# Kernel optimization log

Hardware: AMD Instinct MI355X
Metric: run time of the kernel (lower is better)

The kernel has to match this reference:

```python
import jax, jax.numpy as jnp
import numpy as np

K_ORDER = 3
GRID_N = 10
GRID_LO, GRID_HI = -2.0, 2.0
LAYERS = [(49, 256), (256, 256), (256, 10)]
NCOEF = GRID_N + K_ORDER  # 13


def mish(x):
    return x * jnp.tanh(jax.nn.softplus(x))


def bspline_basis(x):
    # x: (B, in) -> basis (B, in, GRID_N + K_ORDER)
    h = (GRID_HI - GRID_LO) / GRID_N
    knots = GRID_LO + h * jnp.arange(-K_ORDER, GRID_N + K_ORDER + 1, dtype=x.dtype)  # (G+2k+1,)
    xx = x[..., None]
    B = ((xx >= knots[:-1]) & (xx < knots[1:])).astype(x.dtype)  # degree-0, (B,in,G+2k)
    for d in range(1, K_ORDER + 1):
        left = (xx - knots[: -(d + 1)]) / (knots[d:-1] - knots[: -(d + 1)]) * B[..., :-1]
        right = (knots[d + 1:] - xx) / (knots[d + 1:] - knots[1:-d]) * B[..., 1:]
        B = left + right
    return B  # (B, in, G+k)


def kan_layer(x, coef, scale_base, scale_sp, bias):
    # x: (B,in); coef: (in,out,G+k); scales: (in,out); bias: (out,)
    basis = bspline_basis(x)                                   # (B,in,G+k)
    spline = jnp.einsum('big,iog->bo', basis, coef * scale_sp[..., None])
    base = jnp.einsum('bi,io->bo', mish(x), scale_base)
    return base + spline + bias


def setup_inputs() -> dict:
    key = jax.random.key(0)
    ks = jax.random.split(key, 1 + 4 * len(LAYERS))
    inp = {'x': jax.random.normal(ks[0], (8192, 1, 28, 28), dtype=jnp.float32)}
    i = 1
    for li, (fin, fout) in enumerate(LAYERS, start=1):
        inp[f'coef{li}'] = 0.1 * jax.random.normal(ks[i], (fin, fout, NCOEF), dtype=jnp.float32); i += 1
        inp[f'sb{li}'] = 1.0 + 0.1 * jax.random.normal(ks[i], (fin, fout), dtype=jnp.float32); i += 1
        inp[f'sp{li}'] = 1.0 + 0.1 * jax.random.normal(ks[i], (fin, fout), dtype=jnp.float32); i += 1
        inp[f'b{li}'] = jnp.zeros((fout,), dtype=jnp.float32); i += 1
    return inp


def reference(x, coef1, sb1, sp1, b1, coef2, sb2, sp2, b2, coef3, sb3, sp3, b3):
    B = x.shape[0]
    # avg_pool2d(x, 4): 28x28 -> 7x7
    h = x.reshape(B, 1, 7, 4, 7, 4).mean(axis=(3, 5))
    h = h.reshape(B, 49)
    h = kan_layer(h, coef1, sb1, sp1, b1)
    h = kan_layer(h, coef2, sb2, sp2, b2)
    h = kan_layer(h, coef3, sb3, sp3, b3)
    return jax.nn.log_softmax(h, axis=1)
```

## Files before the change

### kernel.cpp

```cpp
#include <hip/hip_runtime.h>
#include <hip/hip_bf16.h>

typedef __bf16 bf16x8_t __attribute__((ext_vector_type(8)));
typedef float f32x4_t __attribute__((ext_vector_type(4)));
using bf16 = __hip_bfloat16;

__device__ __forceinline__ unsigned short f2bf_bits(float v) {
  __hip_bfloat16 h = __float2bfloat16(v);
  return *reinterpret_cast<unsigned short*>(&h);
}

__device__ __forceinline__ float mish_f(float x) {
  float z = __expf(x);
  float n = z * (z + 2.0f);
  float m = x * n / (n + 2.0f);
  return (x > 10.0f) ? x : m;
}

__device__ __forceinline__ void kan_feats28(bf16* dst, float x) {
  unsigned int* d32 = (unsigned int*)dst;
#pragma unroll
  for (int d = 0; d < 7; ++d) d32[d] = 0u;
  float t = (x + 3.2f) * 2.5f;
  if (t >= 0.0f && t < 16.0f) {
    float tf = floorf(t);
    int c = (int)tf;
    float u = t - tf;
    float um = 1.0f - u;
    float u2 = u * u, u3 = u2 * u;
    const float s6 = 1.0f / 6.0f;
    float w0 = um * um * um * s6;
    float w1 = (3.0f * u3 - 6.0f * u2 + 4.0f) * s6;
    float w2 = (-3.0f * u3 + 3.0f * u2 + 3.0f * u + 1.0f) * s6;
    float w3 = u3 * s6;
    int j0 = c - 3;
    if (j0 >= 0)               dst[j0]     = __float2bfloat16(w0);
    if (j0 >= -1 && j0 <= 11)  dst[j0 + 1] = __float2bfloat16(w1);
    if (j0 >= -2 && j0 <= 10)  dst[j0 + 2] = __float2bfloat16(w2);
    if (j0 <= 9)               dst[j0 + 3] = __float2bfloat16(w3);
  }
  dst[13] = __float2bfloat16(mish_f(x));
}

__global__ __launch_bounds__(256) void prep_all(
    const float* __restrict__ c1, const float* __restrict__ sb1, const float* __restrict__ sp1,
    const float* __restrict__ c2, const float* __restrict__ sb2, const float* __restrict__ sp2,
    const float* __restrict__ c3, const float* __restrict__ sb3, const float* __restrict__ sp3,
    bf16* __restrict__ W1f, bf16* __restrict__ W2f, bf16* __restrict__ W3f) {
  const int b = blockIdx.x, t = threadIdx.x;
  float vals[14];
  if (b < 49) {
    const int i = b, o = t;
    const int ntg = o >> 4, lrr = o & 15;
    const size_t io = (size_t)i * 256 + o;
    const float spv = sp1[io];
#pragma unroll
    for (int r = 0; r < 13; ++r) vals[r] = c1[io * 13 + r] * spv;
    vals[13] = sb1[io];
#pragma unroll
    for (int d = 0; d < 7; ++d) {
      const int k2 = i * 14 + 2 * d;
      const int s = k2 >> 5, r2 = k2 & 31;
      const size_t off = ((size_t)(s * 16 + ntg)) * 512 + lrr * 32 + (r2 >> 3) * 8 + (r2 & 7);
      *(unsigned int*)(W1f + off) = (unsigned int)f2bf_bits(vals[2 * d]) |
                                    ((unsigned int)f2bf_bits(vals[2 * d + 1]) << 16);
    }
  } else if (b == 49) {
    const int ntg = t >> 4, lrr = t & 15;
#pragma unroll
    for (int d = 0; d < 9; ++d) {
      const int k2 = 686 + 2 * d;
      const int r2 = k2 & 31;
      *(unsigned int*)(W1f + ((size_t)(21 * 16 + ntg)) * 512 + lrr * 32 + (r2 >> 3) * 8 + (r2 & 7)) = 0u;
    }
  } else if (b < 562) {
    if (t >= 128) return;
    const int idx = b - 50;
    const int i = idx >> 1;
    const int o = (idx & 1) * 128 + t;
    const int ntg = o >> 4, lrr = o & 15;
    const size_t io = (size_t)i * 256 + o;
    const float spv = sp2[io];
#pragma unroll
    for (int r = 0; r < 13; ++r) vals[r] = c2[io * 13 + r] * spv;
    vals[13] = sb2[io];
#pragma unroll
    for (int d = 0; d < 7; ++d) {
      const int k2 = i * 14 + 2 * d;
      const int s = k2 >> 5, r2 = k2 & 31;
      const size_t off = ((size_t)(s * 16 + ntg)) * 512 + lrr * 32 + (r2 >> 3) * 8 + (r2 & 7);
      *(unsigned int*)(W2f + off) = (unsigned int)f2bf_bits(vals[2 * d]) |
                                    ((unsigned int)f2bf_bits(vals[2 * d + 1]) << 16);
    }
  } else {
    const int i = b - 562, o = t;
    if (o < 10) {
      const size_t io = (size_t)i * 10 + o;
      const float spv = sp3[io];
#pragma unroll
      for (int r = 0; r < 13; ++r) vals[r] = c3[io * 13 + r] * spv;
      vals[13] = sb3[io];
#pragma unroll
      for (int d = 0; d < 7; ++d) {
        const int k2 = i * 14 + 2 * d;
        const int s = k2 >> 5, r2 = k2 & 31;
        const size_t off = (size_t)s * 512 + o * 32 + (r2 >> 3) * 8 + (r2 & 7);
        *(unsigned int*)(W3f + off) = (unsigned int)f2bf_bits(vals[2 * d]) |
                                      ((unsigned int)f2bf_bits(vals[2 * d + 1]) << 16);
      }
    } else if (o < 16) {
#pragma unroll
      for (int d = 0; d < 7; ++d) {
        const int k2 = i * 14 + 2 * d;
        const int s = k2 >> 5, r2 = k2 & 31;
        *(unsigned int*)(W3f + (size_t)s * 512 + o * 32 + (r2 >> 3) * 8 + (r2 & 7)) = 0u;
      }
    }
  }
}

__global__ __launch_bounds__(1024, 4) void meganet(
    const float* __restrict__ x, const bf16* __restrict__ W1f,
    const bf16* __restrict__ W2f, const bf16* __restrict__ W3f,
    const float* __restrict__ b1, const float* __restrict__ b2,
    const float* __restrict__ b3, float* __restrict__ out) {
  __shared__ __align__(16) char lds[73728];
  float* const Hs = (float*)lds;
  bf16* const Ach0 = (bf16*)(lds + 36864);
  bf16* const Ach1 = (bf16*)(lds + 51712);
  float* const P = (float*)(lds + 66560);
  float* const xs = (float*)lds;
  float* const Red = (float*)(lds + 36864);
  float* const V = (float*)(lds + 51712);

  const int t = threadIdx.x;
  const int w = t >> 6, lane = t & 63, quad = lane >> 4, lr = lane & 15;
  const int tr = (t >> 4) & 31, ej = t & 15;
  const int r0 = blockIdx.x * 32;
  const int foff = lr * 32 + quad * 8;
  const bool cons = (w < 8);
  const int ntg0 = 2 * w;

  for (int h = 0; h < 2; ++h) {
    const float4* src = (const float4*)x + (size_t)(r0 + h * 16) * 196;
    float4* xd = (float4*)xs;
#pragma unroll
    for (int l = 0; l < 4; ++l) {
      const int idx = t + l * 1024;
      if (idx < 3136) xd[idx] = src[idx];
    }
    __syncthreads();
    if (t < 784) {
      const int img = t / 49, p = t - img * 49;
      const int oh = p / 7, ow = p - oh * 7;
      const float* xi = xs + img * 784 + oh * 112 + ow * 4;
      float s = 0.f;
#pragma unroll
      for (int rr = 0; rr < 4; ++rr)
#pragma unroll
        for (int cc = 0; cc < 4; ++cc) s += xi[rr * 28 + cc];
      P[(h * 16 + img) * 56 + p] = s * (1.0f / 16.0f);
    }
    __syncthreads();
  }

  f32x4_t acc[2][2];
#pragma unroll
  for (int m = 0; m < 2; ++m)
#pragma unroll
    for (int n = 0; n < 2; ++n) acc[m][n] = (f32x4_t){0.f, 0.f, 0.f, 0.f};

  bf16x8_t q0[4], q1[4];
  if (cons) {
#pragma unroll
    for (int s = 0; s < 4; ++s) {
      q0[s] = *(const bf16x8_t*)(W1f + (size_t)(s * 16 + ntg0) * 512 + foff);
      q1[s] = *(const bf16x8_t*)(W1f + (size_t)(s * 16 + ntg0 + 1) * 512 + foff);
    }
  } else {
    kan_feats28(Ach0 + tr * 232 + ej * 14, P[tr * 56 + ej]);
  }
  __syncthreads();
#pragma unroll
  for (int c = 0; c < 4; ++c) {
    const bf16* const Ac = (c & 1) ? Ach1 : Ach0;
    bf16* const An = (c & 1) ? Ach0 : Ach1;
    if (cons) {
      const int nks = (c < 3) ? 7 : 1;
#pragma unroll
      for (int ks = 0; ks < 7; ++ks) {
        if (ks >= nks) continue;
        const int kk = c * 7 + ks;
        const int sl = kk & 3;
        bf16x8_t bb0 = q0[sl], bb1 = q1[sl];
        if (kk + 4 < 22) {
          q0[sl] = *(const bf16x8_t*)(W1f + (size_t)((kk + 4) * 16 + ntg0) * 512 + foff);
          q1[sl] = *(const bf16x8_t*)(W1f + (size_t)((kk + 4) * 16 + ntg0 + 1) * 512 + foff);
        }
#pragma unroll
        for (int m = 0; m < 2; ++m) {
          bf16x8_t a = *(const bf16x8_t*)(Ac + (m * 16 + lr) * 232 + ks * 32 + quad * 8);
          acc[m][0] = __builtin_amdgcn_mfma_f32_16x16x32_bf16(a, bb0, acc[m][0], 0, 0, 0);
          acc[m][1] = __builtin_amdgcn_mfma_f32_16x16x32_bf16(a, bb1, acc[m][1], 0, 0, 0);
        }
      }
    } else {
      if (c < 2) {
        kan_feats28(An + tr * 232 + ej * 14, P[tr * 56 + (c + 1) * 16 + ej]);
      } else if (c == 2) {
        if (ej == 0) kan_feats28(An + tr * 232, P[tr * 56 + 48]);
        else if (ej == 1) {
          unsigned int* z = (unsigned int*)(An + tr * 232 + 14);
#pragma unroll
          for (int d = 0; d < 9; ++d) z[d] = 0u;
        }
      }
    }
    __syncthreads();
  }
  if (cons) {
#pragma unroll
    for (int m = 0; m < 2; ++m)
#pragma unroll
      for (int n = 0; n < 2; ++n) {
        const int col = w * 32 + n * 16 + lr;
        const float bn = b1[col];
        f32x4_t v;
#pragma unroll
        for (int r = 0; r < 4; ++r) v[r] = acc[m][n][r] + bn;
        *(f32x4_t*)(Hs + col * 36 + m * 16 + quad * 4) = v;
      }
  }
  __syncthreads();

#pragma unroll
  for (int m = 0; m < 2; ++m)
#pragma unroll
    for (int n = 0; n < 2; ++n) acc[m][n] = (f32x4_t){0.f, 0.f, 0.f, 0.f};
  if (cons) {
#pragma unroll
    for (int s = 0; s < 4; ++s) {
      q0[s] = *(const bf16x8_t*)(W2f + (size_t)(s * 16 + ntg0) * 512 + foff);
      q1[s] = *(const bf16x8_t*)(W2f + (size_t)(s * 16 + ntg0 + 1) * 512 + foff);
    }
  } else {
    kan_feats28(Ach0 + tr * 232 + ej * 14, Hs[ej * 36 + tr]);
  }
  __syncthreads();
#pragma unroll
  for (int c = 0; c < 16; ++c) {
    const bf16* const Ac = (c & 1) ? Ach1 : Ach0;
    bf16* const An = (c & 1) ? Ach0 : Ach1;
    if (cons) {
#pragma unroll
      for (int ks = 0; ks < 7; ++ks) {
        const int kk = c * 7 + ks;
        const int sl = kk & 3;
        bf16x8_t bb0 = q0[sl], bb1 = q1[sl];
        if (kk + 4 < 112) {
          q0[sl] = *(const bf16x8_t*)(W2f + (size_t)((kk + 4) * 16 + ntg0) * 512 + foff);
          q1[sl] = *(const bf16x8_t*)(W2f + (size_t)((kk + 4) * 16 + ntg0 + 1) * 512 + foff);
        }
#pragma unroll
        for (int m = 0; m < 2; ++m) {
          bf16x8_t a = *(const bf16x8_t*)(Ac + (m * 16 + lr) * 232 + ks * 32 + quad * 8);
          acc[m][0] = __builtin_amdgcn_mfma_f32_16x16x32_bf16(a, bb0, acc[m][0], 0, 0, 0);
          acc[m][1] = __builtin_amdgcn_mfma_f32_16x16x32_bf16(a, bb1, acc[m][1], 0, 0, 0);
        }
      }
    } else if (c < 15) {
      kan_feats28(An + tr * 232 + ej * 14, Hs[((c + 1) * 16 + ej) * 36 + tr]);
    }
    __syncthreads();
  }
  if (cons) {
#pragma unroll
    for (int m = 0; m < 2; ++m)
#pragma unroll
      for (int n = 0; n < 2; ++n) {
        const int col = w * 32 + n * 16 + lr;
        const float bn = b2[col];
        f32x4_t v;
#pragma unroll
        for (int r = 0; r < 4; ++r) v[r] = acc[m][n][r] + bn;
        *(f32x4_t*)(Hs + col * 36 + m * 16 + quad * 4) = v;
      }
  }
  __syncthreads();

  f32x4_t acc3[2];
  acc3[0] = (f32x4_t){0.f, 0.f, 0.f, 0.f};
  acc3[1] = acc3[0];
  bf16x8_t q3[4];
  if (w < 7) {
#pragma unroll
    for (int s = 0; s < 4; ++s)
      q3[s] = *(const bf16x8_t*)(W3f + (size_t)(s * 7 + w) * 512 + foff);
  } else if (!cons) {
    kan_feats28(Ach0 + tr * 232 + ej * 14, Hs[ej * 36 + tr]);
  }
  __syncthreads();
#pragma unroll
  for (int c = 0; c < 16; ++c) {
    const bf16* const Ac = (c & 1) ? Ach1 : Ach0;
    bf16* const An = (c & 1) ? Ach0 : Ach1;
    if (w < 7) {
      bf16x8_t bb = q3[c & 3];
      if (c + 4 < 16)
        q3[c & 3] = *(const bf16x8_t*)(W3f + (size_t)((c + 4) * 7 + w) * 512 + foff);
#pragma unroll
      for (int m = 0; m < 2; ++m) {
        bf16x8_t a = *(const bf16x8_t*)(Ac + (m * 16 + lr) * 232 + w * 32 + quad * 8);
        acc3[m] = __builtin_amdgcn_mfma_f32_16x16x32_bf16(a, bb, acc3[m], 0, 0, 0);
      }
    } else if (!cons && c < 15) {
      kan_feats28(An + tr * 232 + ej * 14, Hs[((c + 1) * 16 + ej) * 36 + tr]);
    }
    __syncthreads();
  }
  if (w < 7) {
#pragma unroll
    for (int m = 0; m < 2; ++m)
#pragma unroll
      for (int r = 0; r < 4; ++r)
        Red[w * 512 + (m * 16 + quad * 4 + r) * 16 + lr] = acc3[m][r];
  }
  __syncthreads();
  if (t < 512) {
    float s = (ej < 10) ? b3[ej] : 0.f;
#pragma unroll
    for (int ks = 0; ks < 7; ++ks) s += Red[ks * 512 + tr * 16 + ej];
    V[tr * 16 + ej] = s;
  }
  __syncthreads();
  if (t < 32) {
    float vv[10];
#pragma unroll
    for (int o = 0; o < 10; ++o) vv[o] = V[t * 16 + o];
    float mx = vv[0];
#pragma unroll
    for (int o = 1; o < 10; ++o) mx = fmaxf(mx, vv[o]);
    float se = 0.f;
#pragma unroll
    for (int o = 0; o < 10; ++o) se += expf(vv[o] - mx);
    const float l = mx + logf(se);
#pragma unroll
    for (int o = 0; o < 10; ++o) out[(size_t)(r0 + t) * 10 + o] = vv[o] - l;
  }
}

extern "C" void kernel_launch(void* const* d_in, const int* in_sizes, int n_in,
                              void* d_out, int out_size, void* d_ws, size_t ws_size,
                              hipStream_t stream) {
  const float* x = (const float*)d_in[0];
  const float* coef1 = (const float*)d_in[1];
  const float* sb1 = (const float*)d_in[2];
  const float* sp1 = (const float*)d_in[3];
  const float* b1 = (const float*)d_in[4];
  const float* coef2 = (const float*)d_in[5];
  const float* sb2 = (const float*)d_in[6];
  const float* sp2 = (const float*)d_in[7];
  const float* b2 = (const float*)d_in[8];
  const float* coef3 = (const float*)d_in[9];
  const float* sb3 = (const float*)d_in[10];
  const float* sp3 = (const float*)d_in[11];
  const float* b3 = (const float*)d_in[12];
  float* out = (float*)d_out;

  char* ws = (char*)d_ws;
  bf16* W1f = (bf16*)ws;
  bf16* W2f = (bf16*)(ws + 360448);
  bf16* W3f = (bf16*)(ws + 2195456);

  prep_all<<<818, 256, 0, stream>>>(coef1, sb1, sp1, coef2, sb2, sp2,
                                    coef3, sb3, sp3, W1f, W2f, W3f);
  meganet<<<256, 1024, 0, stream>>>(x, W1f, W2f, W3f, b1, b2, b3, out);
}
```

Before: 140.3 us.

## Pool input directly from global memory and use lighter barriers with MFMA priority

The input pooling stage now reads each 4x4 window straight from global memory with nontemporal vector loads, replacing the LDS staging and two extra barriers per half-batch. All __syncthreads calls become a custom barrier that waits only on LDS counters, so in-flight global weight prefetches are not drained at every barrier. MFMA consumer waves raise their scheduling priority during the matmul loops. The custom barrier relies on global-load results being waited on elsewhere by the compiler, and setprio could starve the feature-producing waves.

```diff
diff --git a/kernel.cpp b/kernel.cpp
--- a/kernel.cpp
+++ b/kernel.cpp
@@ -15,6 +15,12 @@
   float n = z * (z + 2.0f);
   float m = x * n / (n + 2.0f);
   return (x > 10.0f) ? x : m;
+}
+
+__device__ __forceinline__ void bar() {
+  asm volatile("s_waitcnt lgkmcnt(0)" ::: "memory");
+  __builtin_amdgcn_s_barrier();
+  asm volatile("" ::: "memory");
 }
 
 __device__ __forceinline__ void kan_feats28(bf16* dst, float x) {
@@ -129,7 +135,6 @@
   bf16* const Ach0 = (bf16*)(lds + 36864);
   bf16* const Ach1 = (bf16*)(lds + 51712);
   float* const P = (float*)(lds + 66560);
-  float* const xs = (float*)lds;
   float* const Red = (float*)(lds + 36864);
   float* const V = (float*)(lds + 51712);
 
@@ -141,35 +146,6 @@
   const bool cons = (w < 8);
   const int ntg0 = 2 * w;
 
-  for (int h = 0; h < 2; ++h) {
-    const float4* src = (const float4*)x + (size_t)(r0 + h * 16) * 196;
-    float4* xd = (float4*)xs;
-#pragma unroll
-    for (int l = 0; l < 4; ++l) {
-      const int idx = t + l * 1024;
-      if (idx < 3136) xd[idx] = src[idx];
-    }
-    __syncthreads();
-    if (t < 784) {
-      const int img = t / 49, p = t - img * 49;
-      const int oh = p / 7, ow = p - oh * 7;
-      const float* xi = xs + img * 784 + oh * 112 + ow * 4;
-      float s = 0.f;
-#pragma unroll
-      for (int rr = 0; rr < 4; ++rr)
-#pragma unroll
-        for (int cc = 0; cc < 4; ++cc) s += xi[rr * 28 + cc];
-      P[(h * 16 + img) * 56 + p] = s * (1.0f / 16.0f);
-    }
-    __syncthreads();
-  }
-
-  f32x4_t acc[2][2];
-#pragma unroll
-  for (int m = 0; m < 2; ++m)
-#pragma unroll
-    for (int n = 0; n < 2; ++n) acc[m][n] = (f32x4_t){0.f, 0.f, 0.f, 0.f};
-
   bf16x8_t q0[4], q1[4];
   if (cons) {
 #pragma unroll
@@ -177,15 +153,41 @@
       q0[s] = *(const bf16x8_t*)(W1f + (size_t)(s * 16 + ntg0) * 512 + foff);
       q1[s] = *(const bf16x8_t*)(W1f + (size_t)(s * 16 + ntg0 + 1) * 512 + foff);
     }
-  } else {
-    kan_feats28(Ach0 + tr * 232 + ej * 14, P[tr * 56 + ej]);
-  }
-  __syncthreads();
+  }
+
+  {
+    const float* xb = x + (size_t)r0 * 784;
+#pragma unroll
+    for (int j = t; j < 1568; j += 1024) {
+      const int img = j / 49;
+      const int p = j - img * 49;
+      const int oh = p / 7, ow = p - oh * 7;
+      const float* xi = xb + img * 784 + oh * 112 + ow * 4;
+      const f32x4_t a = __builtin_nontemporal_load((const f32x4_t*)(xi));
+      const f32x4_t b = __builtin_nontemporal_load((const f32x4_t*)(xi + 28));
+      const f32x4_t c = __builtin_nontemporal_load((const f32x4_t*)(xi + 56));
+      const f32x4_t d = __builtin_nontemporal_load((const f32x4_t*)(xi + 84));
+      const float s = (a[0] + a[1] + a[2] + a[3]) + (b[0] + b[1] + b[2] + b[3]) +
+                      (c[0] + c[1] + c[2] + c[3]) + (d[0] + d[1] + d[2] + d[3]);
+      P[img * 56 + p] = s * 0.0625f;
+    }
+  }
+  bar();
+
+  f32x4_t acc[2][2];
+#pragma unroll
+  for (int m = 0; m < 2; ++m)
+#pragma unroll
+    for (int n = 0; n < 2; ++n) acc[m][n] = (f32x4_t){0.f, 0.f, 0.f, 0.f};
+
+  if (!cons) kan_feats28(Ach0 + tr * 232 + ej * 14, P[tr * 56 + ej]);
+  bar();
 #pragma unroll
   for (int c = 0; c < 4; ++c) {
     const bf16* const Ac = (c & 1) ? Ach1 : Ach0;
     bf16* const An = (c & 1) ? Ach0 : Ach1;
     if (cons) {
+      __builtin_amdgcn_s_setprio(1);
       const int nks = (c < 3) ? 7 : 1;
 #pragma unroll
       for (int ks = 0; ks < 7; ++ks) {
@@ -204,6 +206,7 @@
           acc[m][1] = __builtin_amdgcn_mfma_f32_16x16x32_bf16(a, bb1, acc[m][1], 0, 0, 0);
         }
       }
+      __builtin_amdgcn_s_setprio(0);
     } else {
       if (c < 2) {
         kan_feats28(An + tr * 232 + ej * 14, P[tr * 56 + (c + 1) * 16 + ej]);
@@ -216,7 +219,7 @@
         }
       }
     }
-    __syncthreads();
+    bar();
   }
   if (cons) {
 #pragma unroll
@@ -231,7 +234,7 @@
         *(f32x4_t*)(Hs + col * 36 + m * 16 + quad * 4) = v;
       }
   }
-  __syncthreads();
+  bar();
 
 #pragma unroll
   for (int m = 0; m < 2; ++m)
@@ -246,12 +249,13 @@
   } else {
     kan_feats28(Ach0 + tr * 232 + ej * 14, Hs[ej * 36 + tr]);
   }
-  __syncthreads();
+  bar();
 #pragma unroll
   for (int c = 0; c < 16; ++c) {
     const bf16* const Ac = (c & 1) ? Ach1 : Ach0;
     bf16* const An = (c & 1) ? Ach0 : Ach1;
     if (cons) {
+      __builtin_amdgcn_s_setprio(1);
 #pragma unroll
       for (int ks = 0; ks < 7; ++ks) {
         const int kk = c * 7 + ks;
@@ -268,10 +272,11 @@
           acc[m][1] = __builtin_amdgcn_mfma_f32_16x16x32_bf16(a, bb1, acc[m][1], 0, 0, 0);
         }
       }
+      __builtin_amdgcn_s_setprio(0);
     } else if (c < 15) {
       kan_feats28(An + tr * 232 + ej * 14, Hs[((c + 1) * 16 + ej) * 36 + tr]);
     }
-    __syncthreads();
+    bar();
   }
   if (cons) {
 #pragma unroll
@@ -286,7 +291,7 @@
         *(f32x4_t*)(Hs + col * 36 + m * 16 + quad * 4) = v;
       }
   }
-  __syncthreads();
+  bar();
 
   f32x4_t acc3[2];
   acc3[0] = (f32x4_t){0.f, 0.f, 0.f, 0.f};
@@ -299,12 +304,13 @@
   } else if (!cons) {
     kan_feats28(Ach0 + tr * 232 + ej * 14, Hs[ej * 36 + tr]);
   }
-  __syncthreads();
+  bar();
 #pragma unroll
   for (int c = 0; c < 16; ++c) {
     const bf16* const Ac = (c & 1) ? Ach1 : Ach0;
     bf16* const An = (c & 1) ? Ach0 : Ach1;
     if (w < 7) {
+      __builtin_amdgcn_s_setprio(1);
       bf16x8_t bb = q3[c & 3];
       if (c + 4 < 16)
         q3[c & 3] = *(const bf16x8_t*)(W3f + (size_t)((c + 4) * 7 + w) * 512 + foff);
@@ -313,10 +319,11 @@
         bf16x8_t a = *(const bf16x8_t*)(Ac + (m * 16 + lr) * 232 + w * 32 + quad * 8);
         acc3[m] = __builtin_amdgcn_mfma_f32_16x16x32_bf16(a, bb, acc3[m], 0, 0, 0);
       }
+      __builtin_amdgcn_s_setprio(0);
     } else if (!cons && c < 15) {
       kan_feats28(An + tr * 232 + ej * 14, Hs[((c + 1) * 16 + ej) * 36 + tr]);
     }
-    __syncthreads();
+    bar();
   }
   if (w < 7) {
 #pragma unroll
@@ -325,14 +332,14 @@
       for (int r = 0; r < 4; ++r)
         Red[w * 512 + (m * 16 + quad * 4 + r) * 16 + lr] = acc3[m][r];
   }
-  __syncthreads();
+  bar();
   if (t < 512) {
     float s = (ej < 10) ? b3[ej] : 0.f;
 #pragma unroll
     for (int ks = 0; ks < 7; ++ks) s += Red[ks * 512 + tr * 16 + ej];
     V[tr * 16 + ej] = s;
   }
-  __syncthreads();
+  bar();
   if (t < 32) {
     float vv[10];
 #pragma unroll
```

New measurement: 143.0 us. Within noise of the previous version (+1.9%).

## Deepen weight prefetch, use lightweight barriers, make spline feature writes branchless

Applied to the files above, without the earlier changes.

Doubles the register prefetch ring for B-operand weight fragments from 4 to 8 slots. The first layer-1 weights are now issued before the input pooling phase, and the layer-2 weights before the layer-1 epilogue, so global load latency overlaps other work. __syncthreads is replaced by a barrier that only waits on LDS counters (lgkmcnt), which avoids draining outstanding global prefetches at every chunk boundary. kan_feats28 now builds packed 32-bit words with selects instead of zeroing plus conditional scattered stores, and the layer-3 prefetch is moved ahead of the layer-2 epilogue. The costs are higher VGPR pressure, which could reduce occupancy or cause spills, and one extra barrier stage.

```diff
diff --git a/kernel.cpp b/kernel.cpp
--- a/kernel.cpp
+++ b/kernel.cpp
@@ -17,29 +17,44 @@
   return (x > 10.0f) ? x : m;
 }
 
+__device__ __forceinline__ void bar() {
+  asm volatile("s_waitcnt lgkmcnt(0)" ::: "memory");
+  __builtin_amdgcn_s_barrier();
+  asm volatile("" ::: "memory");
+}
+
 __device__ __forceinline__ void kan_feats28(bf16* dst, float x) {
+  float t = (x + 3.2f) * 2.5f;
+  const bool inr = (t >= 0.0f) && (t < 16.0f);
+  float tc = inr ? t : 0.0f;
+  float tf = floorf(tc);
+  const int j0 = (int)tf - 3;
+  float u = tc - tf;
+  float um = 1.0f - u;
+  float u2 = u * u, u3 = u2 * u;
+  const float s6 = 1.0f / 6.0f;
+  float w0 = um * um * um * s6;
+  float w1 = (3.0f * u3 - 6.0f * u2 + 4.0f) * s6;
+  float w2 = (-3.0f * u3 + 3.0f * u2 + 3.0f * u + 1.0f) * s6;
+  float w3 = u3 * s6;
+  if (!inr) { w0 = 0.f; w1 = 0.f; w2 = 0.f; w3 = 0.f; }
+  const unsigned int b0 = f2bf_bits(w0), b1 = f2bf_bits(w1);
+  const unsigned int b2 = f2bf_bits(w2), b3 = f2bf_bits(w3);
+  const unsigned int bm = f2bf_bits(mish_f(x));
   unsigned int* d32 = (unsigned int*)dst;
 #pragma unroll
-  for (int d = 0; d < 7; ++d) d32[d] = 0u;
-  float t = (x + 3.2f) * 2.5f;
-  if (t >= 0.0f && t < 16.0f) {
-    float tf = floorf(t);
-    int c = (int)tf;
-    float u = t - tf;
-    float um = 1.0f - u;
-    float u2 = u * u, u3 = u2 * u;
-    const float s6 = 1.0f / 6.0f;
-    float w0 = um * um * um * s6;
-    float w1 = (3.0f * u3 - 6.0f * u2 + 4.0f) * s6;
-    float w2 = (-3.0f * u3 + 3.0f * u2 + 3.0f * u + 1.0f) * s6;
-    float w3 = u3 * s6;
-    int j0 = c - 3;
-    if (j0 >= 0)               dst[j0]     = __float2bfloat16(w0);
-    if (j0 >= -1 && j0 <= 11)  dst[j0 + 1] = __float2bfloat16(w1);
-    if (j0 >= -2 && j0 <= 10)  dst[j0 + 2] = __float2bfloat16(w2);
-    if (j0 <= 9)               dst[j0 + 3] = __float2bfloat16(w3);
-  }
-  dst[13] = __float2bfloat16(mish_f(x));
+  for (int dd = 0; dd < 7; ++dd) {
+    const int r = 2 * dd - j0;
+    unsigned int lo = (r == 0) ? b0 : (r == 1) ? b1 : (r == 2) ? b2 : (r == 3) ? b3 : 0u;
+    unsigned int hi;
+    if (dd < 6) {
+      const int r1 = r + 1;
+      hi = (r1 == 0) ? b0 : (r1 == 1) ? b1 : (r1 == 2) ? b2 : (r1 == 3) ? b3 : 0u;
+    } else {
+      hi = bm;
+    }
+    d32[dd] = lo | (hi << 16);
+  }
 }
 
 __global__ __launch_bounds__(256) void prep_all(
@@ -141,6 +156,15 @@
   const bool cons = (w < 8);
   const int ntg0 = 2 * w;
 
+  bf16x8_t q0[8], q1[8];
+  if (cons) {
+#pragma unroll
+    for (int s = 0; s < 8; ++s) {
+      q0[s] = *(const bf16x8_t*)(W1f + (size_t)(s * 16 + ntg0) * 512 + foff);
+      q1[s] = *(const bf16x8_t*)(W1f + (size_t)(s * 16 + ntg0 + 1) * 512 + foff);
+    }
+  }
+
   for (int h = 0; h < 2; ++h) {
     const float4* src = (const float4*)x + (size_t)(r0 + h * 16) * 196;
     float4* xd = (float4*)xs;
@@ -149,7 +173,7 @@
       const int idx = t + l * 1024;
       if (idx < 3136) xd[idx] = src[idx];
     }
-    __syncthreads();
+    bar();
     if (t < 784) {
       const int img = t / 49, p = t - img * 49;
       const int oh = p / 7, ow = p - oh * 7;
@@ -161,7 +185,7 @@
         for (int cc = 0; cc < 4; ++cc) s += xi[rr * 28 + cc];
       P[(h * 16 + img) * 56 + p] = s * (1.0f / 16.0f);
     }
-    __syncthreads();
+    bar();
   }
 
   f32x4_t acc[2][2];
@@ -170,17 +194,8 @@
 #pragma unroll
     for (int n = 0; n < 2; ++n) acc[m][n] = (f32x4_t){0.f, 0.f, 0.f, 0.f};
 
-  bf16x8_t q0[4], q1[4];
-  if (cons) {
-#pragma unroll
-    for (int s = 0; s < 4; ++s) {
-      q0[s] = *(const bf16x8_t*)(W1f + (size_t)(s * 16 + ntg0) * 512 + foff);
-      q1[s] = *(const bf16x8_t*)(W1f + (size_t)(s * 16 + ntg0 + 1) * 512 + foff);
-    }
-  } else {
-    kan_feats28(Ach0 + tr * 232 + ej * 14, P[tr * 56 + ej]);
-  }
-  __syncthreads();
+  if (!cons) kan_feats28(Ach0 + tr * 232 + ej * 14, P[tr * 56 + ej]);
+  bar();
 #pragma unroll
   for (int c = 0; c < 4; ++c) {
     const bf16* const Ac = (c & 1) ? Ach1 : Ach0;
@@ -191,11 +206,11 @@
       for (int ks = 0; ks < 7; ++ks) {
         if (ks >= nks) continue;
         const int kk = c * 7 + ks;
-        const int sl = kk & 3;
+        const int sl = kk & 7;
         bf16x8_t bb0 = q0[sl], bb1 = q1[sl];
-        if (kk + 4 < 22) {
-          q0[sl] = *(const bf16x8_t*)(W1f + (size_t)((kk + 4) * 16 + ntg0) * 512 + foff);
-          q1[sl] = *(const bf16x8_t*)(W1f + (size_t)((kk + 4) * 16 + ntg0 + 1) * 512 + foff);
+        if (kk + 8 < 22) {
+          q0[sl] = *(const bf16x8_t*)(W1f + (size_t)((kk + 8) * 16 + ntg0) * 512 + foff);
+          q1[sl] = *(const bf16x8_t*)(W1f + (size_t)((kk + 8) * 16 + ntg0 + 1) * 512 + foff);
         }
 #pragma unroll
         for (int m = 0; m < 2; ++m) {
@@ -216,9 +231,14 @@
         }
       }
     }
-    __syncthreads();
+    bar();
   }
   if (cons) {
+#pragma unroll
+    for (int s = 0; s < 8; ++s) {
+      q0[s] = *(const bf16x8_t*)(W2f + (size_t)(s * 16 + ntg0) * 512 + foff);
+      q1[s] = *(const bf16x8_t*)(W2f + (size_t)(s * 16 + ntg0 + 1) * 512 + foff);
+    }
 #pragma unroll
     for (int m = 0; m < 2; ++m)
 #pragma unroll
@@ -231,22 +251,14 @@
         *(f32x4_t*)(Hs + col * 36 + m * 16 + quad * 4) = v;
       }
   }
-  __syncthreads();
+  bar();
 
 #pragma unroll
   for (int m = 0; m < 2; ++m)
 #pragma unroll
     for (int n = 0; n < 2; ++n) acc[m][n] = (f32x4_t){0.f, 0.f, 0.f, 0.f};
-  if (cons) {
-#pragma unroll
-    for (int s = 0; s < 4; ++s) {
-      q0[s] = *(const bf16x8_t*)(W2f + (size_t)(s * 16 + ntg0) * 512 + foff);
-      q1[s] = *(const bf16x8_t*)(W2f + (size_t)(s * 16 + ntg0 + 1) * 512 + foff);
-    }
-  } else {
-    kan_feats28(Ach0 + tr * 232 + ej * 14, Hs[ej * 36 + tr]);
-  }
-  __syncthreads();
+  if (!cons) kan_feats28(Ach0 + tr * 232 + ej * 14, Hs[ej * 36 + tr]);
+  bar();
 #pragma unroll
   for (int c = 0; c < 16; ++c) {
     const bf16* const Ac = (c & 1) ? Ach1 : Ach0;
@@ -255,11 +267,11 @@
 #pragma unroll
       for (int ks = 0; ks < 7; ++ks) {
         const int kk = c * 7 + ks;
-        const int sl = kk & 3;
+        const int sl = kk & 7;
         bf16x8_t bb0 = q0[sl], bb1 = q1[sl];
-        if (kk + 4 < 112) {
-          q0[sl] = *(const bf16x8_t*)(W2f + (size_t)((kk + 4) * 16 + ntg0) * 512 + foff);
-          q1[sl] = *(const bf16x8_t*)(W2f + (size_t)((kk + 4) * 16 + ntg0 + 1) * 512 + foff);
+        if (kk + 8 < 112) {
+          q0[sl] = *(const bf16x8_t*)(W2f + (size_t)((kk + 8) * 16 + ntg0) * 512 + foff);
+          q1[sl] = *(const bf16x8_t*)(W2f + (size_t)((kk + 8) * 16 + ntg0 + 1) * 512 + foff);
         }
 #pragma unroll
         for (int m = 0; m < 2; ++m) {
@@ -271,22 +283,8 @@
     } else if (c < 15) {
       kan_feats28(An + tr * 232 + ej * 14, Hs[((c + 1) * 16 + ej) * 36 + tr]);
     }
-    __syncthreads();
-  }
-  if (cons) {
-#pragma unroll
-    for (int m = 0; m < 2; ++m)
-#pragma unroll
-      for (int n = 0; n < 2; ++n) {
-        const int col = w * 32 + n * 16 + lr;
-        const float bn = b2[col];
-        f32x4_t v;
-#pragma unroll
-        for (int r = 0; r < 4; ++r) v[r] = acc[m][n][r] + bn;
-        *(f32x4_t*)(Hs + col * 36 + m * 16 + quad * 4) = v;
-      }
-  }
-  __syncthreads();
+    bar();
+  }
 
   f32x4_t acc3[2];
   acc3[0] = (f32x4_t){0.f, 0.f, 0.f, 0.f};
@@ -296,10 +294,24 @@
 #pragma unroll
     for (int s = 0; s < 4; ++s)
       q3[s] = *(const bf16x8_t*)(W3f + (size_t)(s * 7 + w) * 512 + foff);
-  } else if (!cons) {
-    kan_feats28(Ach0 + tr * 232 + ej * 14, Hs[ej * 36 + tr]);
-  }
-  __syncthreads();
+  }
+  if (cons) {
+#pragma unroll
+    for (int m = 0; m < 2; ++m)
+#pragma unroll
+      for (int n = 0; n < 2; ++n) {
+        const int col = w * 32 + n * 16 + lr;
+        const float bn = b2[col];
+        f32x4_t v;
+#pragma unroll
+        for (int r = 0; r < 4; ++r) v[r] = acc[m][n][r] + bn;
+        *(f32x4_t*)(Hs + col * 36 + m * 16 + quad * 4) = v;
+      }
+  }
+  bar();
+
+  if (!cons) kan_feats28(Ach0 + tr * 232 + ej * 14, Hs[ej * 36 + tr]);
+  bar();
 #pragma unroll
   for (int c = 0; c < 16; ++c) {
     const bf16* const Ac = (c & 1) ? Ach1 : Ach0;
@@ -316,7 +328,7 @@
     } else if (!cons && c < 15) {
       kan_feats28(An + tr * 232 + ej * 14, Hs[((c + 1) * 16 + ej) * 36 + tr]);
     }
-    __syncthreads();
+    bar();
   }
   if (w < 7) {
 #pragma unroll
@@ -325,14 +337,14 @@
       for (int r = 0; r < 4; ++r)
         Red[w * 512 + (m * 16 + quad * 4 + r) * 16 + lr] = acc3[m][r];
   }
-  __syncthreads();
+  bar();
   if (t < 512) {
     float s = (ej < 10) ? b3[ej] : 0.f;
 #pragma unroll
     for (int ks = 0; ks < 7; ++ks) s += Red[ks * 512 + tr * 16 + ej];
     V[tr * 16 + ej] = s;
   }
-  __syncthreads();
+  bar();
   if (t < 32) {
     float vv[10];
 #pragma unroll
```

Result: slower. 224.7 us (+60.1%).

## Double the feature chunk per barrier in layers 2-3 and repack prep kernel

Applied to the files above, without the earlier changes.

Layers 2 and 3 now produce spline features for 32 input columns per stage instead of 16, using wider LDS A buffers (row stride 472), so the MFMA loops run 8 stages with half as many __syncthreads. The prep kernel is reshaped to use all 256 threads per block for layer-2 and layer-3 weights, which cuts the grid from 818 to 322 blocks. The avg-pool sum now uses float4 LDS reads. In exchange, LDS use per block rises to about 102 KB, and each producer wave does twice the feature work per stage, which may lengthen the critical path between barriers.

```diff
diff --git a/kernel.cpp b/kernel.cpp
--- a/kernel.cpp
+++ b/kernel.cpp
@@ -73,11 +73,9 @@
       const int r2 = k2 & 31;
       *(unsigned int*)(W1f + ((size_t)(21 * 16 + ntg)) * 512 + lrr * 32 + (r2 >> 3) * 8 + (r2 & 7)) = 0u;
     }
-  } else if (b < 562) {
-    if (t >= 128) return;
-    const int idx = b - 50;
-    const int i = idx >> 1;
-    const int o = (idx & 1) * 128 + t;
+  } else if (b < 306) {
+    const int i = b - 50;
+    const int o = t;
     const int ntg = o >> 4, lrr = o & 15;
     const size_t io = (size_t)i * 256 + o;
     const float spv = sp2[io];
@@ -93,7 +91,8 @@
                                     ((unsigned int)f2bf_bits(vals[2 * d + 1]) << 16);
     }
   } else {
-    const int i = b - 562, o = t;
+    const int idx = (b - 306) * 256 + t;
+    const int i = idx >> 4, o = idx & 15;
     if (o < 10) {
       const size_t io = (size_t)i * 10 + o;
       const float spv = sp3[io];
@@ -108,7 +107,7 @@
         *(unsigned int*)(W3f + off) = (unsigned int)f2bf_bits(vals[2 * d]) |
                                       ((unsigned int)f2bf_bits(vals[2 * d + 1]) << 16);
       }
-    } else if (o < 16) {
+    } else {
 #pragma unroll
       for (int d = 0; d < 7; ++d) {
         const int k2 = i * 14 + 2 * d;
@@ -124,14 +123,14 @@
     const bf16* __restrict__ W2f, const bf16* __restrict__ W3f,
     const float* __restrict__ b1, const float* __restrict__ b2,
     const float* __restrict__ b3, float* __restrict__ out) {
-  __shared__ __align__(16) char lds[73728];
+  __shared__ __align__(16) char lds[104448];
   float* const Hs = (float*)lds;
-  bf16* const Ach0 = (bf16*)(lds + 36864);
-  bf16* const Ach1 = (bf16*)(lds + 51712);
-  float* const P = (float*)(lds + 66560);
+  bf16* const A0 = (bf16*)(lds + 36864);
+  bf16* const A1 = (bf16*)(lds + 67072);
+  float* const P = (float*)(lds + 97280);
   float* const xs = (float*)lds;
   float* const Red = (float*)(lds + 36864);
-  float* const V = (float*)(lds + 51712);
+  float* const V = (float*)(lds + 67072);
 
   const int t = threadIdx.x;
   const int w = t >> 6, lane = t & 63, quad = lane >> 4, lr = lane & 15;
@@ -154,12 +153,13 @@
       const int img = t / 49, p = t - img * 49;
       const int oh = p / 7, ow = p - oh * 7;
       const float* xi = xs + img * 784 + oh * 112 + ow * 4;
-      float s = 0.f;
-#pragma unroll
-      for (int rr = 0; rr < 4; ++rr)
-#pragma unroll
-        for (int cc = 0; cc < 4; ++cc) s += xi[rr * 28 + cc];
-      P[(h * 16 + img) * 56 + p] = s * (1.0f / 16.0f);
+      f32x4_t s4 = (f32x4_t){0.f, 0.f, 0.f, 0.f};
+#pragma unroll
+      for (int rr = 0; rr < 4; ++rr) {
+        const f32x4_t v = *(const f32x4_t*)(xi + rr * 28);
+        s4 += v;
+      }
+      P[(h * 16 + img) * 56 + p] = (s4[0] + s4[1] + s4[2] + s4[3]) * (1.0f / 16.0f);
     }
     __syncthreads();
   }
@@ -170,6 +170,8 @@
 #pragma unroll
     for (int n = 0; n < 2; ++n) acc[m][n] = (f32x4_t){0.f, 0.f, 0.f, 0.f};
 
+  bf16* const Bch0 = A0;
+  bf16* const Bch1 = A1;
   bf16x8_t q0[4], q1[4];
   if (cons) {
 #pragma unroll
@@ -178,13 +180,13 @@
       q1[s] = *(const bf16x8_t*)(W1f + (size_t)(s * 16 + ntg0 + 1) * 512 + foff);
     }
   } else {
-    kan_feats28(Ach0 + tr * 232 + ej * 14, P[tr * 56 + ej]);
+    kan_feats28(Bch0 + tr * 232 + ej * 14, P[tr * 56 + ej]);
   }
   __syncthreads();
 #pragma unroll
   for (int c = 0; c < 4; ++c) {
-    const bf16* const Ac = (c & 1) ? Ach1 : Ach0;
-    bf16* const An = (c & 1) ? Ach0 : Ach1;
+    const bf16* const Ac = (c & 1) ? Bch1 : Bch0;
+    bf16* const An = (c & 1) ? Bch0 : Bch1;
     if (cons) {
       const int nks = (c < 3) ? 7 : 1;
 #pragma unroll
@@ -244,17 +246,18 @@
       q1[s] = *(const bf16x8_t*)(W2f + (size_t)(s * 16 + ntg0 + 1) * 512 + foff);
     }
   } else {
-    kan_feats28(Ach0 + tr * 232 + ej * 14, Hs[ej * 36 + tr]);
-  }
-  __syncthreads();
-#pragma unroll
-  for (int c = 0; c < 16; ++c) {
-    const bf16* const Ac = (c & 1) ? Ach1 : Ach0;
-    bf16* const An = (c & 1) ? Ach0 : Ach1;
+    kan_feats28(A0 + tr * 472 + ej * 14, Hs[ej * 36 + tr]);
+    kan_feats28(A0 + tr * 472 + (16 + ej) * 14, Hs[(16 + ej) * 36 + tr]);
+  }
+  __syncthreads();
+#pragma unroll
+  for (int S = 0; S < 8; ++S) {
+    const bf16* const Ac = (S & 1) ? A1 : A0;
+    bf16* const An = (S & 1) ? A0 : A1;
     if (cons) {
 #pragma unroll
-      for (int ks = 0; ks < 7; ++ks) {
-        const int kk = c * 7 + ks;
+      for (int ks = 0; ks < 14; ++ks) {
+        const int kk = S * 14 + ks;
         const int sl = kk & 3;
         bf16x8_t bb0 = q0[sl], bb1 = q1[sl];
         if (kk + 4 < 112) {
@@ -263,13 +266,15 @@
         }
 #pragma unroll
         for (int m = 0; m < 2; ++m) {
-          bf16x8_t a = *(const bf16x8_t*)(Ac + (m * 16 + lr) * 232 + ks * 32 + quad * 8);
+          bf16x8_t a = *(const bf16x8_t*)(Ac + (m * 16 + lr) * 472 + ks * 32 + quad * 8);
           acc[m][0] = __builtin_amdgcn_mfma_f32_16x16x32_bf16(a, bb0, acc[m][0], 0, 0, 0);
           acc[m][1] = __builtin_amdgcn_mfma_f32_16x16x32_bf16(a, bb1, acc[m][1], 0, 0, 0);
         }
       }
-    } else if (c < 15) {
-      kan_feats28(An + tr * 232 + ej * 14, Hs[((c + 1) * 16 + ej) * 36 + tr]);
+    } else if (S < 7) {
+      const int col = 32 * (S + 1);
+      kan_feats28(An + tr * 472 + ej * 14, Hs[(col + ej) * 36 + tr]);
+      kan_feats28(An + tr * 472 + (16 + ej) * 14, Hs[(col + 16 + ej) * 36 + tr]);
     }
     __syncthreads();
   }
@@ -297,24 +302,39 @@
     for (int s = 0; s < 4; ++s)
       q3[s] = *(const bf16x8_t*)(W3f + (size_t)(s * 7 + w) * 512 + foff);
   } else if (!cons) {
-    kan_feats28(Ach0 + tr * 232 + ej * 14, Hs[ej * 36 + tr]);
-  }
-  __syncthreads();
-#pragma unroll
-  for (int c = 0; c < 16; ++c) {
-    const bf16* const Ac = (c & 1) ? Ach1 : Ach0;
-    bf16* const An = (c & 1) ? Ach0 : Ach1;
+    kan_feats28(A0 + tr * 472 + ej * 14, Hs[ej * 36 + tr]);
+    kan_feats28(A0 + tr * 472 + (16 + ej) * 14, Hs[(16 + ej) * 36 + tr]);
+  }
+  __syncthreads();
+#pragma unroll
+  for (int S = 0; S < 8; ++S) {
+    const bf16* const Ac = (S & 1) ? A1 : A0;
+    bf16* const An = (S & 1) ? A0 : A1;
     if (w < 7) {
-      bf16x8_t bb = q3[c & 3];
-      if (c + 4 < 16)
-        q3[c & 3] = *(const bf16x8_t*)(W3f + (size_t)((c + 4) * 7 + w) * 512 + foff);
-#pragma unroll
-      for (int m = 0; m < 2; ++m) {
-        bf16x8_t a = *(const bf16x8_t*)(Ac + (m * 16 + lr) * 232 + w * 32 + quad * 8);
-        acc3[m] = __builtin_amdgcn_mfma_f32_16x16x32_bf16(a, bb, acc3[m], 0, 0, 0);
-      }
-    } else if (!cons && c < 15) {
-      kan_feats28(An + tr * 232 + ej * 14, Hs[((c + 1) * 16 + ej) * 36 + tr]);
+      {
+        const int c0 = 2 * S;
+        bf16x8_t bb = q3[c0 & 3];
+        if (c0 + 4 < 16)
+          q3[c0 & 3] = *(const bf16x8_t*)(W3f + (size_t)((c0 + 4) * 7 + w) * 512 + foff);
+        bf16x8_t a0 = *(const bf16x8_t*)(Ac + lr * 472 + w * 32 + quad * 8);
+        bf16x8_t a1 = *(const bf16x8_t*)(Ac + (16 + lr) * 472 + w * 32 + quad * 8);
+        acc3[0] = __builtin_amdgcn_mfma_f32_16x16x32_bf16(a0, bb, acc3[0], 0, 0, 0);
+        acc3[1] = __builtin_amdgcn_mfma_f32_16x16x32_bf16(a1, bb, acc3[1], 0, 0, 0);
+      }
+      {
+        const int c1 = 2 * S + 1;
+        bf16x8_t bb = q3[c1 & 3];
+        if (c1 + 4 < 16)
+          q3[c1 & 3] = *(const bf16x8_t*)(W3f + (size_t)((c1 + 4) * 7 + w) * 512 + foff);
+        bf16x8_t a0 = *(const bf16x8_t*)(Ac + lr * 472 + (w + 7) * 32 + quad * 8);
+        bf16x8_t a1 = *(const bf16x8_t*)(Ac + (16 + lr) * 472 + (w + 7) * 32 + quad * 8);
+        acc3[0] = __builtin_amdgcn_mfma_f32_16x16x32_bf16(a0, bb, acc3[0], 0, 0, 0);
+        acc3[1] = __builtin_amdgcn_mfma_f32_16x16x32_bf16(a1, bb, acc3[1], 0, 0, 0);
+      }
+    } else if (!cons && S < 7) {
+      const int col = 32 * (S + 1);
+      kan_feats28(An + tr * 472 + ej * 14, Hs[(col + ej) * 36 + tr]);
+      kan_feats28(An + tr * 472 + (16 + ej) * 14, Hs[(col + 16 + ej) * 36 + tr]);
     }
     __syncthreads();
   }
@@ -372,7 +392,7 @@
   bf16* W2f = (bf16*)(ws + 360448);
   bf16* W3f = (bf16*)(ws + 2195456);
 
-  prep_all<<<818, 256, 0, stream>>>(coef1, sb1, sp1, coef2, sb2, sp2,
+  prep_all<<<322, 256, 0, stream>>>(coef1, sb1, sp1, coef2, sb2, sp2,
                                     coef3, sb3, sp3, W1f, W2f, W3f);
   meganet<<<256, 1024, 0, stream>>>(x, W1f, W2f, W3f, b1, b2, b3, out);
 }
```

Result: no change. 138.4 us (median of 2 runs) (-1.3%).
